# Performance work log

Hardware: AMD Instinct MI355X
Metric: run time of the kernel (lower is better)

## Reference

```python
import jax, jax.numpy as jnp
import numpy as np

PI = float(np.pi)


def _layernorm(x, g, b, eps=1e-5):
    mu = jnp.mean(x, axis=-1, keepdims=True)
    var = jnp.var(x, axis=-1, keepdims=True)
    return (x - mu) * jax.lax.rsqrt(var + eps) * g + b


def setup_inputs() -> dict:
    key = jax.random.key(0)
    B, L, D, P = 4, 2048, 256, 32
    ks = jax.random.split(key, 16)

    def lin_w(k, fi, fo):
        return (jax.random.normal(k, (fi, fo), dtype=jnp.float32) / np.sqrt(fi)).astype(jnp.float32)

    inp = {
        'x': jax.random.normal(ks[0], (B, L, D), dtype=jnp.float32),
        'pos_phases': jax.random.normal(ks[1], (L, P), dtype=jnp.float32) * PI,
        'w_mem1v': lin_w(ks[2], D, P), 'b_mem1v': jnp.zeros((P,), jnp.float32),
        'w_mem1o': lin_w(ks[3], P, D), 'b_mem1o': jnp.zeros((D,), jnp.float32),
        'w_off': lin_w(ks[4], D + P, P), 'b_off': jnp.zeros((P,), jnp.float32),
        'w_key': lin_w(ks[5], D, P), 'b_key': jnp.zeros((P,), jnp.float32),
        'w_val': lin_w(ks[6], D, D), 'b_val': jnp.zeros((D,), jnp.float32),
        'w_sk1': lin_w(ks[7], 2 * D, D), 'b_sk1': jnp.zeros((D,), jnp.float32),
        'w_sk2': lin_w(ks[8], D, P), 'b_sk2': jnp.zeros((P,), jnp.float32),
        'w_gate': lin_w(ks[9], D, 1), 'b_gate': jnp.zeros((1,), jnp.float32),
        'ln_g': jnp.ones((D,), jnp.float32), 'ln_b': jnp.zeros((D,), jnp.float32),
        'w_out': lin_w(ks[10], D, D), 'b_out': jnp.zeros((D,), jnp.float32),
    }
    return inp


def reference(x, pos_phases, w_mem1v, b_mem1v, w_mem1o, b_mem1o, w_off, b_off,
              w_key, b_key, w_val, b_val, w_sk1, b_sk1, w_sk2, b_sk2,
              w_gate, b_gate, ln_g, ln_b, w_out, b_out):
    B, L, D = x.shape
    P = pos_phases.shape[-1]

    pos_cos = jnp.cos(pos_phases)  # [L,P]
    pos_sin = jnp.sin(pos_phases)

    # Memory 1: flat [B,L,P] phasor cumulative memory
    v1 = x @ w_mem1v + b_mem1v                       # [B,L,P]
    mem1_cos = jnp.cumsum(pos_cos[None] * v1, axis=1)
    mem1_sin = jnp.cumsum(pos_sin[None] * v1, axis=1)

    offset_input = jnp.concatenate([x, jnp.broadcast_to(pos_phases[None], (B, L, P))], axis=-1)
    offset = jnp.tanh(offset_input @ w_off + b_off) * PI
    oc, os = jnp.cos(offset), jnp.sin(offset)
    query_cos = pos_cos[None] * oc - pos_sin[None] * os
    query_sin = pos_sin[None] * oc + pos_cos[None] * os
    pos_ret = (mem1_cos * query_cos + mem1_sin * query_sin) / np.sqrt(P)
    pos_out = pos_ret @ w_mem1o + b_mem1o            # [B,L,D]

    # Memory 2: full [B,L,P,D] phasor KV cumulative memory
    key_phases = jnp.tanh(x @ w_key + b_key) * PI    # [B,L,P]
    key_cos, key_sin = jnp.cos(key_phases), jnp.sin(key_phases)
    values = x @ w_val + b_val                       # [B,L,D]
    store_gate = jax.nn.sigmoid(x @ w_gate + b_gate) # [B,L,1]

    positions = jnp.arange(1, L + 1, dtype=x.dtype)[None, :, None]
    context_avg = jnp.cumsum(x, axis=1) / positions
    h = jax.nn.gelu(jnp.concatenate([x, context_avg], axis=-1) @ w_sk1 + b_sk1, approximate=False)
    storage_phases = jnp.tanh(h @ w_sk2 + b_sk2) * PI  # [B,L,P]

    gated_v = values * store_gate                    # [B,L,D]
    kv_mem_cos = jnp.cumsum(jnp.cos(storage_phases)[..., None] * gated_v[:, :, None, :], axis=1)  # [B,L,P,D]
    kv_mem_sin = jnp.cumsum(jnp.sin(storage_phases)[..., None] * gated_v[:, :, None, :], axis=1)

    gate_cumsum = jnp.clip(jnp.cumsum(store_gate, axis=1), 1.0, None)  # [B,L,1]
    kv_retrieved = jnp.einsum('blpd,blp->bld', kv_mem_cos, key_cos) + \
                   jnp.einsum('blpd,blp->bld', kv_mem_sin, key_sin)
    kv_retrieved = kv_retrieved / (jnp.sqrt(gate_cumsum) * np.sqrt(P))

    combined = pos_out + kv_retrieved
    return x + _layernorm(combined, ln_g, ln_b) @ w_out + b_out
```

## Files before the change

kernel.cpp:

```cpp
#include <hip/hip_runtime.h>
#include <hip/hip_bf16.h>

constexpr int B_ = 4;
constexpr int L_ = 2048;
constexpr int D_ = 256;
constexpr int P_ = 32;
constexpr int CL = 32;
constexpr int NC = L_ / CL;

#define PI_F 3.14159265358979323846f
#define INV_SQRT_P 0.17677669529663687f

typedef __attribute__((ext_vector_type(8))) short short8_t;
typedef __attribute__((ext_vector_type(4))) float floatx4;

static __device__ inline short f2bf(float f) {
  unsigned int u;
  __builtin_memcpy(&u, &f, 4);
  unsigned int r = (u + 0x7fffu + ((u >> 16) & 1u)) >> 16;
  return (short)r;
}
static __device__ inline float bf2f(short s) {
  unsigned int u = ((unsigned int)(unsigned short)s) << 16;
  float f;
  __builtin_memcpy(&f, &u, 4);
  return f;
}

__global__ void wprep(const float* __restrict__ x, const float* __restrict__ pos,
                      const float* __restrict__ w_val, const float* __restrict__ w_mem1v,
                      const float* __restrict__ w_off, const float* __restrict__ b_off,
                      const float* __restrict__ w_key, const float* __restrict__ w_gate,
                      const float* __restrict__ w_sk1, const float* __restrict__ w_out,
                      const float* __restrict__ w_sk2, const float* __restrict__ w_mem1o,
                      short* __restrict__ WA, short* __restrict__ W1,
                      short* __restrict__ WO, short* __restrict__ W2T,
                      short* __restrict__ W1OT,
                      short* __restrict__ xbf, float* __restrict__ poff,
                      float* __restrict__ ctxsum) {
  __shared__ float2 psum[2][128];
  int blk = blockIdx.x, tid = threadIdx.x;
  if (blk < 384) {
    int idx = blk * 256 + tid;
    int n = idx >> 8, k = idx & 255;
    float v;
    if (n < 256) v = w_val[k * 256 + n];
    else if (n < 288) v = w_mem1v[k * 32 + (n - 256)];
    else if (n < 320) v = w_off[k * 32 + (n - 288)];
    else if (n < 352) v = w_key[k * 32 + (n - 320)];
    else if (n == 352) v = w_gate[k];
    else v = 0.f;
    WA[idx] = f2bf(v);
  } else if (blk < 896) {
    int idx = (blk - 384) * 256 + tid;
    int n = idx >> 9, k = idx & 511;
    W1[idx] = f2bf(w_sk1[k * 256 + n]);
  } else if (blk < 1152) {
    int idx = (blk - 896) * 256 + tid;
    int n = idx >> 8, k = idx & 255;
    WO[idx] = f2bf(w_out[k * 256 + n]);
  } else if (blk < 1184) {
    int idx = (blk - 1152) * 256 + tid;
    int p = idx >> 8, k = idx & 255;
    W2T[idx] = f2bf(w_sk2[k * 32 + p]);
  } else if (blk < 1216) {
    int idx = (blk - 1184) * 256 + tid;
    int d = idx >> 5, p = idx & 31;
    W1OT[idx] = f2bf(w_mem1o[p * 256 + d]);
  } else if (blk < 1472) {
    int idx = (blk - 1216) * 256 + tid;
    int l = idx >> 5, p = idx & 31;
    float a = b_off[p];
#pragma unroll 8
    for (int j = 0; j < 32; ++j) a += pos[l * 32 + j] * w_off[(256 + j) * 32 + p];
    poff[idx] = a;
  } else {
    int c2 = blk - 1472;
    int b = c2 >> 6, ch = c2 & 63;
    int d2 = (tid & 127) * 2, h = tid >> 7;
    int tokb = b * L_ + ch * 32 + h * 16;
    float2 xv[16];
#pragma unroll
    for (int i = 0; i < 16; ++i)
      xv[i] = *(const float2*)&x[(tokb + i) * 256 + d2];
    float2 s = {0.f, 0.f};
#pragma unroll
    for (int i = 0; i < 16; ++i) { s.x += xv[i].x; s.y += xv[i].y; }
#pragma unroll
    for (int i = 0; i < 16; ++i) {
      short2 o;
      o.x = f2bf(xv[i].x);
      o.y = f2bf(xv[i].y);
      *(short2*)&xbf[(tokb + i) * 256 + d2] = o;
    }
    psum[h][tid & 127] = s;
    __syncthreads();
    if (h == 0) {
      float2 o = psum[1][tid & 127];
      float2 tot = {s.x + o.x, s.y + o.y};
      *(float2*)&ctxsum[c2 * 256 + d2] = tot;
    }
  }
}

__global__ __launch_bounds__(384, 3) void gemmA3(const short* __restrict__ xbf,
                                                 const short* __restrict__ WA,
                                                 const float* __restrict__ pos,
                                                 const float* __restrict__ poff,
                                                 const float* __restrict__ b_mem1v,
                                                 const float* __restrict__ b_key,
                                                 const float* __restrict__ b_gate,
                                                 const float* __restrict__ b_val,
                                                 float* __restrict__ m1cT,
                                                 float* __restrict__ m1sT,
                                                 float* __restrict__ qc,
                                                 float* __restrict__ qs,
                                                 short* __restrict__ K2bf,
                                                 short* __restrict__ gvT,
                                                 float* __restrict__ sg) {
  __shared__ float YL[16][132];
  __shared__ float gsh[16];
  int tid = threadIdx.x;
  int lane = tid & 63, w = tid >> 6;
  int ml = lane & 15, quad = lane >> 4, kq = quad * 8;
  int bc = blockIdx.x;
  int bc32 = bc >> 1, half = bc & 1;
  int tok0 = bc * 16;
  floatx4 acc[4] = {};
  const short* A0p = &xbf[(tok0 + ml) * 256 + kq];
  const short* Bp = &WA[(w * 64 + ml) * 256 + kq];
#pragma unroll
  for (int ks = 0; ks < 8; ++ks) {
    short8_t a0 = *(const short8_t*)(A0p + ks * 32);
#pragma unroll
    for (int nt = 0; nt < 4; ++nt) {
      short8_t b = *(const short8_t*)(Bp + nt * 16 * 256 + ks * 32);
      acc[nt] = __builtin_amdgcn_mfma_f32_16x16x32_bf16(a0, b, acc[nt], 0, 0, 0);
    }
  }
  if (w >= 4) {
#pragma unroll
    for (int nt = 0; nt < 4; ++nt) {
      int col = (w - 4) * 64 + nt * 16 + ml;
#pragma unroll
      for (int r = 0; r < 4; ++r)
        YL[quad * 4 + r][col] = acc[nt][r];
    }
  }
  __syncthreads();
  if (tid < 256) {
#pragma unroll
    for (int it = 0; it < 2; ++it) {
      int idx = it * 256 + tid;
      int t = idx >> 5, p = idx & 31;
      int tok = tok0 + t, l = tok & (L_ - 1);
      int b = tok >> 11;
      float v1 = YL[t][p] + b_mem1v[p];
      float ph = pos[l * 32 + p];
      float pc = cosf(ph), ps = sinf(ph);
      int idxT = (b * 32 + p) * L_ + l;
      m1cT[idxT] = pc * v1;
      m1sT[idxT] = ps * v1;
      float off = tanhf(YL[t][32 + p] + poff[l * 32 + p]) * PI_F;
      float oc = cosf(off), os = sinf(off);
      int gidx = tok * 32 + p;
      qc[gidx] = pc * oc - ps * os;
      qs[gidx] = ps * oc + pc * os;
      float kp = tanhf(YL[t][64 + p] + b_key[p]) * PI_F;
      K2bf[tok * 64 + p] = f2bf(cosf(kp));
      K2bf[tok * 64 + 32 + p] = f2bf(sinf(kp));
      if (p == 0) {
        float g = 1.f / (1.f + expf(-(YL[t][96] + b_gate[0])));
        sg[tok] = g;
        gsh[t] = g;
      }
    }
  }
  __syncthreads();
  if (w < 4) {
#pragma unroll
    for (int nt = 0; nt < 4; ++nt) {
      int d = w * 64 + nt * 16 + ml;
      float bv = b_val[d];
      int t0 = quad * 4;
      short4 o;
      o.x = f2bf((acc[nt][0] + bv) * gsh[t0 + 0]);
      o.y = f2bf((acc[nt][1] + bv) * gsh[t0 + 1]);
      o.z = f2bf((acc[nt][2] + bv) * gsh[t0 + 2]);
      o.w = f2bf((acc[nt][3] + bv) * gsh[t0 + 3]);
      *(short4*)&gvT[(bc32 * 256 + d) * 32 + half * 16 + t0] = o;
    }
  }
}

__global__ void scan_all(float* __restrict__ m1cT, float* __restrict__ m1sT,
                         float* __restrict__ sg) {
  __shared__ float wsum[4];
  int blk = blockIdx.x;
  int tid = threadIdx.x;
  int lane = tid & 63, w = tid >> 6;
  float* arr;
  int base;
  if (blk < 256) {
    arr = (blk < 128) ? m1cT : m1sT;
    base = (blk & 127) * L_;
  } else {
    arr = sg;
    base = (blk - 256) * L_;
  }
  int sbase = base + w * 512;
  float v[8];
#pragma unroll
  for (int i = 0; i < 8; ++i) v[i] = arr[sbase + i * 64 + lane];
  float carry = 0.f;
#pragma unroll
  for (int i = 0; i < 8; ++i) {
    float vv = v[i];
#pragma unroll
    for (int off = 1; off < 64; off <<= 1) {
      float n = __shfl_up(vv, off, 64);
      if (lane >= off) vv += n;
    }
    vv += carry;
    v[i] = vv;
    carry = __shfl(vv, 63, 64);
  }
  if (lane == 0) wsum[w] = carry;
  __syncthreads();
  float off = 0.f;
  for (int ww = 0; ww < w; ++ww) off += wsum[ww];
#pragma unroll
  for (int i = 0; i < 8; ++i) arr[sbase + i * 64 + lane] = v[i] + off;
}

union __align__(16) CDMem {
  short As[32][520];
  struct { short HS[32][280]; short SPL[64][40]; } h;
};
__global__ __launch_bounds__(512, 4) void gemmCD(const short* __restrict__ xbf,
                                                 const float* __restrict__ x,
                                                 const float* __restrict__ ctxsum,
                                                 const short* __restrict__ W1,
                                                 const float* __restrict__ b_sk1,
                                                 const short* __restrict__ W2T,
                                                 const float* __restrict__ b_sk2,
                                                 const short* __restrict__ gvT,
                                                 short* __restrict__ SPbf,
                                                 short* __restrict__ UT) {
  __shared__ CDMem sm;
  __shared__ float stmp[256];
  int tid = threadIdx.x;
  int bc = blockIdx.x;
  int tok0 = bc * 32;
  int bI = bc >> 6, ch = bc & 63;
  int lane = tid & 63, w = tid >> 6;
  int ml = lane & 15, quad = lane >> 4, kq = quad * 8;
#pragma unroll
  for (int pass = 0; pass < 2; ++pass) {
    int idx = pass * 512 + tid;
    int row = idx >> 5, c8 = idx & 31;
    *(short8_t*)&sm.As[row][c8 * 8] =
        *(const short8_t*)&xbf[(tok0 + row) * 256 + c8 * 8];
  }
  {
    int d = tid & 255, h = tid >> 8;
    float cp = 0.f;
    int sb = bI * 64 * 256 + d;
    int c = 0;
    for (; c + 8 <= ch; c += 8) {
      float t0 = ctxsum[sb + (c + 0) * 256];
      float t1 = ctxsum[sb + (c + 1) * 256];
      float t2 = ctxsum[sb + (c + 2) * 256];
      float t3 = ctxsum[sb + (c + 3) * 256];
      float t4 = ctxsum[sb + (c + 4) * 256];
      float t5 = ctxsum[sb + (c + 5) * 256];
      float t6 = ctxsum[sb + (c + 6) * 256];
      float t7 = ctxsum[sb + (c + 7) * 256];
      cp += ((t0 + t1) + (t2 + t3)) + ((t4 + t5) + (t6 + t7));
    }
    for (; c < ch; ++c) cp += ctxsum[sb + c * 256];
    float xv[16];
    int xb = (tok0 + h * 16) * 256 + d;
#pragma unroll
    for (int i = 0; i < 16; ++i) xv[i] = x[xb + i * 256];
    float p = 0.f;
#pragma unroll
    for (int i = 0; i < 16; ++i) p += xv[i];
    if (h == 0) stmp[d] = p;
    __syncthreads();
    float run = cp + (h ? stmp[d] : 0.f);
    int l0 = ch * 32 + h * 16;
#pragma unroll
    for (int i = 0; i < 16; ++i) {
      run += xv[i];
      sm.As[h * 16 + i][256 + d] = f2bf(run / (float)(l0 + i + 1));
    }
  }
  __syncthreads();
  int n0w = w * 32;
  floatx4 acc[2][2] = {};
#pragma unroll
  for (int kt = 0; kt < 16; ++kt) {
    short8_t a0 = *(short8_t*)&sm.As[ml][kt * 32 + kq];
    short8_t a1 = *(short8_t*)&sm.As[16 + ml][kt * 32 + kq];
    short8_t b0 = *(const short8_t*)&W1[(n0w + ml) * 512 + kt * 32 + kq];
    short8_t b1 = *(const short8_t*)&W1[(n0w + 16 + ml) * 512 + kt * 32 + kq];
    acc[0][0] = __builtin_amdgcn_mfma_f32_16x16x32_bf16(a0, b0, acc[0][0], 0, 0, 0);
    acc[0][1] = __builtin_amdgcn_mfma_f32_16x16x32_bf16(a0, b1, acc[0][1], 0, 0, 0);
    acc[1][0] = __builtin_amdgcn_mfma_f32_16x16x32_bf16(a1, b0, acc[1][0], 0, 0, 0);
    acc[1][1] = __builtin_amdgcn_mfma_f32_16x16x32_bf16(a1, b1, acc[1][1], 0, 0, 0);
  }
  short hv[2][2][4];
#pragma unroll
  for (int nt = 0; nt < 2; ++nt) {
    float bv = b_sk1[n0w + nt * 16 + ml];
#pragma unroll
    for (int mt = 0; mt < 2; ++mt)
#pragma unroll
      for (int r = 0; r < 4; ++r) {
        float v = acc[mt][nt][r] + bv;
        float g = 0.5f * v * (1.f + erff(v * 0.70710678118654752f));
        hv[mt][nt][r] = f2bf(g);
      }
  }
  __syncthreads();
#pragma unroll
  for (int mt = 0; mt < 2; ++mt)
#pragma unroll
    for (int nt = 0; nt < 2; ++nt)
#pragma unroll
      for (int r = 0; r < 4; ++r)
        sm.h.HS[mt * 16 + quad * 4 + r][n0w + nt * 16 + ml] = hv[mt][nt][r];
  __syncthreads();
  if (w < 4) {
    int th = w & 1, ph = w >> 1;
    floatx4 pacc = {};
#pragma unroll
    for (int s = 0; s < 8; ++s) {
      short8_t a = *(short8_t*)&sm.h.HS[th * 16 + ml][s * 32 + kq];
      short8_t b0 = *(const short8_t*)&W2T[(ph * 16 + ml) * 256 + s * 32 + kq];
      pacc = __builtin_amdgcn_mfma_f32_16x16x32_bf16(a, b0, pacc, 0, 0, 0);
    }
    int p = ph * 16 + ml;
    float bs = b_sk2[p];
#pragma unroll
    for (int r = 0; r < 4; ++r) {
      int tl = th * 16 + quad * 4 + r;
      int tok = tok0 + tl;
      float sp = tanhf(pacc[r] + bs) * PI_F;
      short c = f2bf(cosf(sp)), s2 = f2bf(sinf(sp));
      sm.h.SPL[p][tl] = c;
      sm.h.SPL[32 + p][tl] = s2;
      SPbf[tok * 64 + p] = c;
      SPbf[tok * 64 + 32 + p] = s2;
    }
  }
  __syncthreads();
  short8_t a[4];
#pragma unroll
  for (int mt = 0; mt < 4; ++mt) a[mt] = *(short8_t*)&sm.h.SPL[mt * 16 + ml][kq];
  floatx4 acc3[4][2] = {};
#pragma unroll
  for (int nt = 0; nt < 2; ++nt) {
    int d = w * 32 + nt * 16 + ml;
    short8_t b = *(const short8_t*)&gvT[(bc * 256 + d) * 32 + kq];
#pragma unroll
    for (int mt = 0; mt < 4; ++mt)
      acc3[mt][nt] = __builtin_amdgcn_mfma_f32_16x16x32_bf16(a[mt], b, acc3[mt][nt], 0, 0, 0);
  }
#pragma unroll
  for (int mt = 0; mt < 4; ++mt)
#pragma unroll
    for (int nt = 0; nt < 2; ++nt) {
      int d = w * 32 + nt * 16 + ml;
      short4 o;
      o.x = f2bf(acc3[mt][nt][0]);
      o.y = f2bf(acc3[mt][nt][1]);
      o.z = f2bf(acc3[mt][nt][2]);
      o.w = f2bf(acc3[mt][nt][3]);
      *(short4*)&UT[(bc * 256 + d) * 64 + mt * 16 + quad * 4] = o;
    }
}

__global__ void kernelE(short* __restrict__ UT) {
  int t = blockIdx.x * 256 + threadIdx.x;
  int pi = t >> 1, half = t & 1;
  int q = pi & 63;
  int d = (pi >> 6) & 255;
  int b = pi >> 14;
  const int cs = 256 * 64;
  int base = ((b * NC) * 256 + d) * 64 + q + half * 32 * cs;
  short v[32];
#pragma unroll
  for (int c = 0; c < 32; ++c) v[c] = UT[base + c * cs];
  float tot = 0.f;
#pragma unroll
  for (int c = 0; c < 32; ++c) tot += bf2f(v[c]);
  float other = __shfl_xor(tot, 1, 64);
  float run = half ? other : 0.f;
#pragma unroll
  for (int c = 0; c < 32; ++c) {
    UT[base + c * cs] = f2bf(run);
    run += bf2f(v[c]);
  }
}

struct __align__(16) FGMem {
  short SL[32][40];
  short PR[32][40];
  float CMB[32][260];
  short CBN[32][280];
  float LG[256], LB[256];
  float scl[32], mu_s[32], rs_s[32];
};
__global__ __launch_bounds__(512, 4) void fgOut(const short* __restrict__ UT,
                                                const short* __restrict__ SPbf,
                                                const short* __restrict__ K2bf,
                                                const short* __restrict__ gvT,
                                                const float* __restrict__ sgc,
                                                const float* __restrict__ m1cT,
                                                const float* __restrict__ m1sT,
                                                const float* __restrict__ qc,
                                                const float* __restrict__ qs,
                                                const short* __restrict__ W1OT,
                                                const float* __restrict__ b_mem1o,
                                                const float* __restrict__ ln_g,
                                                const float* __restrict__ ln_b,
                                                const short* __restrict__ WO,
                                                const float* __restrict__ b_out,
                                                const float* __restrict__ x,
                                                float* __restrict__ out) {
  __shared__ FGMem sm;
  int tid5 = threadIdx.x;
  int bc = blockIdx.x;
  int lbase = bc * CL;
  int bb = bc >> 6, lloc = (bc & 63) * 32;
  int lane = tid5 & 63, w = tid5 >> 6;
  int ml = lane & 15, quad = lane >> 4, kq = quad * 8;
  int d0 = w * 32;
  if (tid5 < 32) sm.scl[tid5] = rsqrtf(fmaxf(sgc[lbase + tid5], 1.f)) * INV_SQRT_P;
  if (tid5 >= 256) {
    int d = tid5 - 256;
    sm.LG[d] = ln_g[d];
    sm.LB[d] = ln_b[d];
  }
  short8_t ka0 = *(const short8_t*)&K2bf[(lbase + ml) * 64 + kq];
  short8_t ka1 = *(const short8_t*)&K2bf[(lbase + 16 + ml) * 64 + kq];
  short8_t kb0 = *(const short8_t*)&K2bf[(lbase + ml) * 64 + 32 + kq];
  short8_t kb1 = *(const short8_t*)&K2bf[(lbase + 16 + ml) * 64 + 32 + kq];
  if (w == 0) {
    floatx4 sacc[2][2] = {};
#pragma unroll
    for (int ks2 = 0; ks2 < 2; ++ks2) {
      short8_t a0 = (ks2 == 0) ? ka0 : kb0;
      short8_t a1 = (ks2 == 0) ? ka1 : kb1;
      short8_t b0 = *(const short8_t*)&SPbf[(lbase + ml) * 64 + ks2 * 32 + kq];
      short8_t b1 = *(const short8_t*)&SPbf[(lbase + 16 + ml) * 64 + ks2 * 32 + kq];
      sacc[0][0] = __builtin_amdgcn_mfma_f32_16x16x32_bf16(a0, b0, sacc[0][0], 0, 0, 0);
      sacc[0][1] = __builtin_amdgcn_mfma_f32_16x16x32_bf16(a0, b1, sacc[0][1], 0, 0, 0);
      sacc[1][0] = __builtin_amdgcn_mfma_f32_16x16x32_bf16(a1, b0, sacc[1][0], 0, 0, 0);
      sacc[1][1] = __builtin_amdgcn_mfma_f32_16x16x32_bf16(a1, b1, sacc[1][1], 0, 0, 0);
    }
#pragma unroll
    for (int mt = 0; mt < 2; ++mt)
#pragma unroll
      for (int nt = 0; nt < 2; ++nt)
#pragma unroll
        for (int r = 0; r < 4; ++r) {
          int trow = mt * 16 + quad * 4 + r;
          int scol = nt * 16 + ml;
          float v = (scol <= trow) ? sacc[mt][nt][r] : 0.f;
          sm.SL[trow][scol] = f2bf(v);
        }
  } else {
    int t7 = tid5 - 64;
    for (int i = t7; i < 1024; i += 448) {
      int pp = i >> 5, t = i & 31;
      int gT = (bb * 32 + pp) * L_ + lloc + t;
      int g = (lbase + t) * 32 + pp;
      sm.PR[t][pp] = f2bf((m1cT[gT] * qc[g] + m1sT[gT] * qs[g]) * INV_SQRT_P);
    }
  }
  __syncthreads();
  floatx4 acc[2][2] = {};
#pragma unroll
  for (int nt = 0; nt < 2; ++nt) {
    short8_t b0 = *(const short8_t*)&UT[(bc * 256 + d0 + nt * 16 + ml) * 64 + kq];
    short8_t b1 = *(const short8_t*)&UT[(bc * 256 + d0 + nt * 16 + ml) * 64 + 32 + kq];
    acc[0][nt] = __builtin_amdgcn_mfma_f32_16x16x32_bf16(ka0, b0, acc[0][nt], 0, 0, 0);
    acc[1][nt] = __builtin_amdgcn_mfma_f32_16x16x32_bf16(ka1, b0, acc[1][nt], 0, 0, 0);
    acc[0][nt] = __builtin_amdgcn_mfma_f32_16x16x32_bf16(kb0, b1, acc[0][nt], 0, 0, 0);
    acc[1][nt] = __builtin_amdgcn_mfma_f32_16x16x32_bf16(kb1, b1, acc[1][nt], 0, 0, 0);
  }
  {
    short8_t a0 = *(short8_t*)&sm.SL[ml][kq];
    short8_t a1 = *(short8_t*)&sm.SL[16 + ml][kq];
#pragma unroll
    for (int nt = 0; nt < 2; ++nt) {
      short8_t b = *(const short8_t*)&gvT[(bc * 256 + d0 + nt * 16 + ml) * 32 + kq];
      acc[0][nt] = __builtin_amdgcn_mfma_f32_16x16x32_bf16(a0, b, acc[0][nt], 0, 0, 0);
      acc[1][nt] = __builtin_amdgcn_mfma_f32_16x16x32_bf16(a1, b, acc[1][nt], 0, 0, 0);
    }
  }
  floatx4 macc[2][2] = {};
  {
    short8_t a0 = *(short8_t*)&sm.PR[ml][kq];
    short8_t a1 = *(short8_t*)&sm.PR[16 + ml][kq];
#pragma unroll
    for (int nt = 0; nt < 2; ++nt) {
      short8_t b = *(const short8_t*)&W1OT[(d0 + nt * 16 + ml) * 32 + kq];
      macc[0][nt] = __builtin_amdgcn_mfma_f32_16x16x32_bf16(a0, b, macc[0][nt], 0, 0, 0);
      macc[1][nt] = __builtin_amdgcn_mfma_f32_16x16x32_bf16(a1, b, macc[1][nt], 0, 0, 0);
    }
  }
#pragma unroll
  for (int mt = 0; mt < 2; ++mt)
#pragma unroll
    for (int nt = 0; nt < 2; ++nt) {
      int d = d0 + nt * 16 + ml;
      float bm = b_mem1o[d];
#pragma unroll
      for (int r = 0; r < 4; ++r) {
        int t = mt * 16 + quad * 4 + r;
        sm.CMB[t][d] = acc[mt][nt][r] * sm.scl[t] + macc[mt][nt][r] + bm;
      }
    }
  __syncthreads();
  {
    int t = tid5 >> 4, g = tid5 & 15;
    float s = 0.f, s2 = 0.f;
#pragma unroll
    for (int j = 0; j < 16; ++j) {
      float v = sm.CMB[t][g + j * 16];
      s += v;
      s2 += v * v;
    }
#pragma unroll
    for (int m = 1; m < 16; m <<= 1) {
      s += __shfl_xor(s, m, 64);
      s2 += __shfl_xor(s2, m, 64);
    }
    if (g == 0) {
      float mu = s / (float)D_;
      float var = s2 / (float)D_ - mu * mu;
      sm.mu_s[t] = mu;
      sm.rs_s[t] = rsqrtf(var + 1e-5f);
    }
  }
  __syncthreads();
#pragma unroll
  for (int it = 0; it < 16; ++it) {
    int i = it * 512 + tid5;
    int t = i >> 8, d = i & 255;
    sm.CBN[t][d] = f2bf((sm.CMB[t][d] - sm.mu_s[t]) * sm.rs_s[t] * sm.LG[d] + sm.LB[d]);
  }
  __syncthreads();
  floatx4 acc2[2][2] = {};
#pragma unroll
  for (int kt = 0; kt < 8; ++kt) {
    short8_t a0 = *(short8_t*)&sm.CBN[ml][kt * 32 + kq];
    short8_t a1 = *(short8_t*)&sm.CBN[16 + ml][kt * 32 + kq];
#pragma unroll
    for (int nt = 0; nt < 2; ++nt) {
      short8_t b = *(const short8_t*)&WO[(d0 + nt * 16 + ml) * 256 + kt * 32 + kq];
      acc2[0][nt] = __builtin_amdgcn_mfma_f32_16x16x32_bf16(a0, b, acc2[0][nt], 0, 0, 0);
      acc2[1][nt] = __builtin_amdgcn_mfma_f32_16x16x32_bf16(a1, b, acc2[1][nt], 0, 0, 0);
    }
  }
#pragma unroll
  for (int nt = 0; nt < 2; ++nt) {
    int n = d0 + nt * 16 + ml;
    float bv = b_out[n];
#pragma unroll
    for (int mt = 0; mt < 2; ++mt)
#pragma unroll
      for (int r = 0; r < 4; ++r) {
        int tok = lbase + mt * 16 + quad * 4 + r;
        out[tok * 256 + n] = x[tok * 256 + n] + acc2[mt][nt][r] + bv;
      }
  }
}

extern "C" void kernel_launch(void* const* d_in, const int* in_sizes, int n_in,
                              void* d_out, int out_size, void* d_ws, size_t ws_size,
                              hipStream_t stream) {
  const float* x = (const float*)d_in[0];
  const float* pos = (const float*)d_in[1];
  const float* w_mem1v = (const float*)d_in[2];
  const float* b_mem1v = (const float*)d_in[3];
  const float* w_mem1o = (const float*)d_in[4];
  const float* b_mem1o = (const float*)d_in[5];
  const float* w_off = (const float*)d_in[6];
  const float* b_off = (const float*)d_in[7];
  const float* w_key = (const float*)d_in[8];
  const float* b_key = (const float*)d_in[9];
  const float* w_val = (const float*)d_in[10];
  const float* b_val = (const float*)d_in[11];
  const float* w_sk1 = (const float*)d_in[12];
  const float* b_sk1 = (const float*)d_in[13];
  const float* w_sk2 = (const float*)d_in[14];
  const float* b_sk2 = (const float*)d_in[15];
  const float* w_gate = (const float*)d_in[16];
  const float* b_gate = (const float*)d_in[17];
  const float* ln_g = (const float*)d_in[18];
  const float* ln_b = (const float*)d_in[19];
  const float* w_out = (const float*)d_in[20];
  const float* b_out = (const float*)d_in[21];
  float* out = (float*)d_out;
  float* ws = (float*)d_ws;

  const int BLP = B_ * L_ * P_;
  const int BLD = B_ * L_ * D_;
  float* m1cT = ws;
  float* m1sT = m1cT + BLP;
  float* qc = m1sT + BLP;
  float* qs = qc + BLP;
  float* sg = qs + BLP;
  float* poff = sg + B_ * L_;
  float* ctxsum = poff + L_ * P_;
  short* UT = (short*)(ctxsum + B_ * 64 * 256);
  short* xbf = UT + (size_t)B_ * NC * 256 * 64;
  short* ctxbf = xbf + BLD;
  short* hs = ctxbf + BLD;
  short* gvT = hs + BLD;
  short* K2bf = gvT + BLD;
  short* SPbf = K2bf + B_ * L_ * 64;
  short* WA = SPbf + B_ * L_ * 64;
  short* W1 = WA + 384 * 256;
  short* WO = W1 + 256 * 512;
  short* W2T = WO + 256 * 256;
  short* W1OT = W2T + 32 * 256;

  wprep<<<1728, 256, 0, stream>>>(x, pos, w_val, w_mem1v, w_off, b_off, w_key, w_gate,
                                  w_sk1, w_out, w_sk2, w_mem1o, WA, W1, WO, W2T, W1OT,
                                  xbf, poff, ctxsum);
  gemmA3<<<512, 384, 0, stream>>>(xbf, WA, pos, poff, b_mem1v, b_key, b_gate, b_val,
                                  m1cT, m1sT, qc, qs, K2bf, gvT, sg);
  gemmCD<<<256, 512, 0, stream>>>(xbf, x, ctxsum, W1, b_sk1, W2T, b_sk2, gvT, SPbf, UT);
  kernelE<<<512, 256, 0, stream>>>(UT);
  scan_all<<<260, 256, 0, stream>>>(m1cT, m1sT, sg);
  fgOut<<<256, 512, 0, stream>>>(UT, SPbf, K2bf, gvT, sg, m1cT, m1sT, qc, qs,
                                 W1OT, b_mem1o, ln_g, ln_b, WO, b_out, x, out);
}
```

Measured before the change: 168.7 us.

## Double threads per block across kernels and pre-scan chunk context sums

gemmA3, gemmCD and fgOut each use twice as many waves, with every wave covering half as many output columns. kernelE now splits each prefix over four lanes instead of two. The serial loop in gemmCD that summed preceding chunk totals is replaced by an exclusive scan of ctxsum, done in extra blocks of scan_all, which now runs before gemmCD. The aim is more parallelism and latency hiding on a grid of only 256–512 blocks, at the cost of less register reuse per wave and heavier 1024-thread blocks.

New measurement: 166.1 us. About the same (-1.5%).

```diff
diff --git a/kernel.cpp b/kernel.cpp
--- a/kernel.cpp
+++ b/kernel.cpp
@@ -103,7 +103,7 @@
   }
 }
 
-__global__ __launch_bounds__(384, 3) void gemmA3(const short* __restrict__ xbf,
+__global__ __launch_bounds__(768, 6) void gemmA3(const short* __restrict__ xbf,
                                                  const short* __restrict__ WA,
                                                  const float* __restrict__ pos,
                                                  const float* __restrict__ poff,
@@ -126,61 +126,57 @@
   int bc = blockIdx.x;
   int bc32 = bc >> 1, half = bc & 1;
   int tok0 = bc * 16;
-  floatx4 acc[4] = {};
+  floatx4 acc[2] = {};
   const short* A0p = &xbf[(tok0 + ml) * 256 + kq];
-  const short* Bp = &WA[(w * 64 + ml) * 256 + kq];
+  const short* Bp = &WA[(w * 32 + ml) * 256 + kq];
 #pragma unroll
   for (int ks = 0; ks < 8; ++ks) {
     short8_t a0 = *(const short8_t*)(A0p + ks * 32);
 #pragma unroll
-    for (int nt = 0; nt < 4; ++nt) {
+    for (int nt = 0; nt < 2; ++nt) {
       short8_t b = *(const short8_t*)(Bp + nt * 16 * 256 + ks * 32);
       acc[nt] = __builtin_amdgcn_mfma_f32_16x16x32_bf16(a0, b, acc[nt], 0, 0, 0);
     }
   }
-  if (w >= 4) {
-#pragma unroll
-    for (int nt = 0; nt < 4; ++nt) {
-      int col = (w - 4) * 64 + nt * 16 + ml;
+  if (w >= 8) {
+#pragma unroll
+    for (int nt = 0; nt < 2; ++nt) {
+      int col = (w - 8) * 32 + nt * 16 + ml;
 #pragma unroll
       for (int r = 0; r < 4; ++r)
         YL[quad * 4 + r][col] = acc[nt][r];
     }
   }
   __syncthreads();
-  if (tid < 256) {
-#pragma unroll
-    for (int it = 0; it < 2; ++it) {
-      int idx = it * 256 + tid;
-      int t = idx >> 5, p = idx & 31;
-      int tok = tok0 + t, l = tok & (L_ - 1);
-      int b = tok >> 11;
-      float v1 = YL[t][p] + b_mem1v[p];
-      float ph = pos[l * 32 + p];
-      float pc = cosf(ph), ps = sinf(ph);
-      int idxT = (b * 32 + p) * L_ + l;
-      m1cT[idxT] = pc * v1;
-      m1sT[idxT] = ps * v1;
-      float off = tanhf(YL[t][32 + p] + poff[l * 32 + p]) * PI_F;
-      float oc = cosf(off), os = sinf(off);
-      int gidx = tok * 32 + p;
-      qc[gidx] = pc * oc - ps * os;
-      qs[gidx] = ps * oc + pc * os;
-      float kp = tanhf(YL[t][64 + p] + b_key[p]) * PI_F;
-      K2bf[tok * 64 + p] = f2bf(cosf(kp));
-      K2bf[tok * 64 + 32 + p] = f2bf(sinf(kp));
-      if (p == 0) {
-        float g = 1.f / (1.f + expf(-(YL[t][96] + b_gate[0])));
-        sg[tok] = g;
-        gsh[t] = g;
-      }
-    }
-  }
-  __syncthreads();
-  if (w < 4) {
-#pragma unroll
-    for (int nt = 0; nt < 4; ++nt) {
-      int d = w * 64 + nt * 16 + ml;
+  if (tid < 512) {
+    int t = tid >> 5, p = tid & 31;
+    int tok = tok0 + t, l = tok & (L_ - 1);
+    int b = tok >> 11;
+    float v1 = YL[t][p] + b_mem1v[p];
+    float ph = pos[l * 32 + p];
+    float pc = cosf(ph), ps = sinf(ph);
+    int idxT = (b * 32 + p) * L_ + l;
+    m1cT[idxT] = pc * v1;
+    m1sT[idxT] = ps * v1;
+    float off = tanhf(YL[t][32 + p] + poff[l * 32 + p]) * PI_F;
+    float oc = cosf(off), os = sinf(off);
+    int gidx = tok * 32 + p;
+    qc[gidx] = pc * oc - ps * os;
+    qs[gidx] = ps * oc + pc * os;
+    float kp = tanhf(YL[t][64 + p] + b_key[p]) * PI_F;
+    K2bf[tok * 64 + p] = f2bf(cosf(kp));
+    K2bf[tok * 64 + 32 + p] = f2bf(sinf(kp));
+    if (p == 0) {
+      float g = 1.f / (1.f + expf(-(YL[t][96] + b_gate[0])));
+      sg[tok] = g;
+      gsh[t] = g;
+    }
+  }
+  __syncthreads();
+  if (w < 8) {
+#pragma unroll
+    for (int nt = 0; nt < 2; ++nt) {
+      int d = w * 32 + nt * 16 + ml;
       float bv = b_val[d];
       int t0 = quad * 4;
       short4 o;
@@ -194,10 +190,24 @@
 }
 
 __global__ void scan_all(float* __restrict__ m1cT, float* __restrict__ m1sT,
-                         float* __restrict__ sg) {
-  __shared__ float wsum[4];
+                         float* __restrict__ sg, float* __restrict__ ctxsum) {
   int blk = blockIdx.x;
   int tid = threadIdx.x;
+  if (blk >= 260) {
+    int b = blk - 260;
+    int base = b * 64 * 256 + tid;
+    float v[64];
+#pragma unroll
+    for (int c = 0; c < 64; ++c) v[c] = ctxsum[base + c * 256];
+    float run = 0.f;
+#pragma unroll
+    for (int c = 0; c < 64; ++c) {
+      ctxsum[base + c * 256] = run;
+      run += v[c];
+    }
+    return;
+  }
+  __shared__ float wsum[4];
   int lane = tid & 63, w = tid >> 6;
   float* arr;
   int base;
@@ -237,100 +247,79 @@
   short As[32][520];
   struct { short HS[32][280]; short SPL[64][40]; } h;
 };
-__global__ __launch_bounds__(512, 4) void gemmCD(const short* __restrict__ xbf,
-                                                 const float* __restrict__ x,
-                                                 const float* __restrict__ ctxsum,
-                                                 const short* __restrict__ W1,
-                                                 const float* __restrict__ b_sk1,
-                                                 const short* __restrict__ W2T,
-                                                 const float* __restrict__ b_sk2,
-                                                 const short* __restrict__ gvT,
-                                                 short* __restrict__ SPbf,
-                                                 short* __restrict__ UT) {
+__global__ __launch_bounds__(1024, 4) void gemmCD(const short* __restrict__ xbf,
+                                                  const float* __restrict__ x,
+                                                  const float* __restrict__ ctxsum,
+                                                  const short* __restrict__ W1,
+                                                  const float* __restrict__ b_sk1,
+                                                  const short* __restrict__ W2T,
+                                                  const float* __restrict__ b_sk2,
+                                                  const short* __restrict__ gvT,
+                                                  short* __restrict__ SPbf,
+                                                  short* __restrict__ UT) {
   __shared__ CDMem sm;
-  __shared__ float stmp[256];
+  __shared__ float stmp[4][256];
   int tid = threadIdx.x;
   int bc = blockIdx.x;
   int tok0 = bc * 32;
   int bI = bc >> 6, ch = bc & 63;
   int lane = tid & 63, w = tid >> 6;
   int ml = lane & 15, quad = lane >> 4, kq = quad * 8;
-#pragma unroll
-  for (int pass = 0; pass < 2; ++pass) {
-    int idx = pass * 512 + tid;
-    int row = idx >> 5, c8 = idx & 31;
+  {
+    int row = tid >> 5, c8 = tid & 31;
     *(short8_t*)&sm.As[row][c8 * 8] =
         *(const short8_t*)&xbf[(tok0 + row) * 256 + c8 * 8];
   }
   {
-    int d = tid & 255, h = tid >> 8;
-    float cp = 0.f;
-    int sb = bI * 64 * 256 + d;
-    int c = 0;
-    for (; c + 8 <= ch; c += 8) {
-      float t0 = ctxsum[sb + (c + 0) * 256];
-      float t1 = ctxsum[sb + (c + 1) * 256];
-      float t2 = ctxsum[sb + (c + 2) * 256];
-      float t3 = ctxsum[sb + (c + 3) * 256];
-      float t4 = ctxsum[sb + (c + 4) * 256];
-      float t5 = ctxsum[sb + (c + 5) * 256];
-      float t6 = ctxsum[sb + (c + 6) * 256];
-      float t7 = ctxsum[sb + (c + 7) * 256];
-      cp += ((t0 + t1) + (t2 + t3)) + ((t4 + t5) + (t6 + t7));
-    }
-    for (; c < ch; ++c) cp += ctxsum[sb + c * 256];
-    float xv[16];
-    int xb = (tok0 + h * 16) * 256 + d;
-#pragma unroll
-    for (int i = 0; i < 16; ++i) xv[i] = x[xb + i * 256];
+    int d = tid & 255, qh = tid >> 8;
+    float cp = ctxsum[(bI * 64 + ch) * 256 + d];
+    float xv[8];
+    int xb = (tok0 + qh * 8) * 256 + d;
+#pragma unroll
+    for (int i = 0; i < 8; ++i) xv[i] = x[xb + i * 256];
     float p = 0.f;
 #pragma unroll
-    for (int i = 0; i < 16; ++i) p += xv[i];
-    if (h == 0) stmp[d] = p;
+    for (int i = 0; i < 8; ++i) p += xv[i];
+    stmp[qh][d] = p;
     __syncthreads();
-    float run = cp + (h ? stmp[d] : 0.f);
-    int l0 = ch * 32 + h * 16;
-#pragma unroll
-    for (int i = 0; i < 16; ++i) {
+    float run = cp;
+    for (int j = 0; j < qh; ++j) run += stmp[j][d];
+    int l0 = ch * 32 + qh * 8;
+#pragma unroll
+    for (int i = 0; i < 8; ++i) {
       run += xv[i];
-      sm.As[h * 16 + i][256 + d] = f2bf(run / (float)(l0 + i + 1));
-    }
-  }
-  __syncthreads();
-  int n0w = w * 32;
-  floatx4 acc[2][2] = {};
+      sm.As[qh * 8 + i][256 + d] = f2bf(run / (float)(l0 + i + 1));
+    }
+  }
+  __syncthreads();
+  int n0w = w * 16;
+  floatx4 acc[2] = {};
 #pragma unroll
   for (int kt = 0; kt < 16; ++kt) {
     short8_t a0 = *(short8_t*)&sm.As[ml][kt * 32 + kq];
     short8_t a1 = *(short8_t*)&sm.As[16 + ml][kt * 32 + kq];
     short8_t b0 = *(const short8_t*)&W1[(n0w + ml) * 512 + kt * 32 + kq];
-    short8_t b1 = *(const short8_t*)&W1[(n0w + 16 + ml) * 512 + kt * 32 + kq];
-    acc[0][0] = __builtin_amdgcn_mfma_f32_16x16x32_bf16(a0, b0, acc[0][0], 0, 0, 0);
-    acc[0][1] = __builtin_amdgcn_mfma_f32_16x16x32_bf16(a0, b1, acc[0][1], 0, 0, 0);
-    acc[1][0] = __builtin_amdgcn_mfma_f32_16x16x32_bf16(a1, b0, acc[1][0], 0, 0, 0);
-    acc[1][1] = __builtin_amdgcn_mfma_f32_16x16x32_bf16(a1, b1, acc[1][1], 0, 0, 0);
-  }
-  short hv[2][2][4];
-#pragma unroll
-  for (int nt = 0; nt < 2; ++nt) {
-    float bv = b_sk1[n0w + nt * 16 + ml];
+    acc[0] = __builtin_amdgcn_mfma_f32_16x16x32_bf16(a0, b0, acc[0], 0, 0, 0);
+    acc[1] = __builtin_amdgcn_mfma_f32_16x16x32_bf16(a1, b0, acc[1], 0, 0, 0);
+  }
+  short hv[2][4];
+  {
+    float bv = b_sk1[n0w + ml];
 #pragma unroll
     for (int mt = 0; mt < 2; ++mt)
 #pragma unroll
       for (int r = 0; r < 4; ++r) {
-        float v = acc[mt][nt][r] + bv;
+        float v = acc[mt][r] + bv;
         float g = 0.5f * v * (1.f + erff(v * 0.70710678118654752f));
-        hv[mt][nt][r] = f2bf(g);
+        hv[mt][r] = f2bf(g);
       }
   }
   __syncthreads();
 #pragma unroll
   for (int mt = 0; mt < 2; ++mt)
 #pragma unroll
-    for (int nt = 0; nt < 2; ++nt)
-#pragma unroll
-      for (int r = 0; r < 4; ++r)
-        sm.h.HS[mt * 16 + quad * 4 + r][n0w + nt * 16 + ml] = hv[mt][nt][r];
+    for (int r = 0; r < 4; ++r)
+      sm.h.HS[mt * 16 + quad * 4 + r][n0w + ml] = hv[mt][r];
   __syncthreads();
   if (w < 4) {
     int th = w & 1, ph = w >> 1;
@@ -359,47 +348,48 @@
   short8_t a[4];
 #pragma unroll
   for (int mt = 0; mt < 4; ++mt) a[mt] = *(short8_t*)&sm.h.SPL[mt * 16 + ml][kq];
-  floatx4 acc3[4][2] = {};
-#pragma unroll
-  for (int nt = 0; nt < 2; ++nt) {
-    int d = w * 32 + nt * 16 + ml;
+  floatx4 acc3[4] = {};
+  {
+    int d = w * 16 + ml;
     short8_t b = *(const short8_t*)&gvT[(bc * 256 + d) * 32 + kq];
 #pragma unroll
     for (int mt = 0; mt < 4; ++mt)
-      acc3[mt][nt] = __builtin_amdgcn_mfma_f32_16x16x32_bf16(a[mt], b, acc3[mt][nt], 0, 0, 0);
-  }
-#pragma unroll
-  for (int mt = 0; mt < 4; ++mt)
-#pragma unroll
-    for (int nt = 0; nt < 2; ++nt) {
-      int d = w * 32 + nt * 16 + ml;
-      short4 o;
-      o.x = f2bf(acc3[mt][nt][0]);
-      o.y = f2bf(acc3[mt][nt][1]);
-      o.z = f2bf(acc3[mt][nt][2]);
-      o.w = f2bf(acc3[mt][nt][3]);
-      *(short4*)&UT[(bc * 256 + d) * 64 + mt * 16 + quad * 4] = o;
-    }
+      acc3[mt] = __builtin_amdgcn_mfma_f32_16x16x32_bf16(a[mt], b, acc3[mt], 0, 0, 0);
+  }
+#pragma unroll
+  for (int mt = 0; mt < 4; ++mt) {
+    int d = w * 16 + ml;
+    short4 o;
+    o.x = f2bf(acc3[mt][0]);
+    o.y = f2bf(acc3[mt][1]);
+    o.z = f2bf(acc3[mt][2]);
+    o.w = f2bf(acc3[mt][3]);
+    *(short4*)&UT[(bc * 256 + d) * 64 + mt * 16 + quad * 4] = o;
+  }
 }
 
 __global__ void kernelE(short* __restrict__ UT) {
   int t = blockIdx.x * 256 + threadIdx.x;
-  int pi = t >> 1, half = t & 1;
+  int pi = t >> 2, j = t & 3;
   int q = pi & 63;
   int d = (pi >> 6) & 255;
   int b = pi >> 14;
   const int cs = 256 * 64;
-  int base = ((b * NC) * 256 + d) * 64 + q + half * 32 * cs;
-  short v[32];
-#pragma unroll
-  for (int c = 0; c < 32; ++c) v[c] = UT[base + c * cs];
+  int base = ((b * NC) * 256 + d) * 64 + q + j * 16 * cs;
+  short v[16];
+#pragma unroll
+  for (int c = 0; c < 16; ++c) v[c] = UT[base + c * cs];
   float tot = 0.f;
 #pragma unroll
-  for (int c = 0; c < 32; ++c) tot += bf2f(v[c]);
-  float other = __shfl_xor(tot, 1, 64);
-  float run = half ? other : 0.f;
-#pragma unroll
-  for (int c = 0; c < 32; ++c) {
+  for (int c = 0; c < 16; ++c) tot += bf2f(v[c]);
+  int lane = threadIdx.x & 63;
+  int gb = lane & ~3;
+  float t0 = __shfl(tot, gb + 0, 64);
+  float t1 = __shfl(tot, gb + 1, 64);
+  float t2 = __shfl(tot, gb + 2, 64);
+  float run = (j > 0 ? t0 : 0.f) + (j > 1 ? t1 : 0.f) + (j > 2 ? t2 : 0.f);
+#pragma unroll
+  for (int c = 0; c < 16; ++c) {
     UT[base + c * cs] = f2bf(run);
     run += bf2f(v[c]);
   }
@@ -413,23 +403,23 @@
   float LG[256], LB[256];
   float scl[32], mu_s[32], rs_s[32];
 };
-__global__ __launch_bounds__(512, 4) void fgOut(const short* __restrict__ UT,
-                                                const short* __restrict__ SPbf,
-                                                const short* __restrict__ K2bf,
-                                                const short* __restrict__ gvT,
-                                                const float* __restrict__ sgc,
-                                                const float* __restrict__ m1cT,
-                                                const float* __restrict__ m1sT,
-                                                const float* __restrict__ qc,
-                                                const float* __restrict__ qs,
-                                                const short* __restrict__ W1OT,
-                                                const float* __restrict__ b_mem1o,
-                                                const float* __restrict__ ln_g,
-                                                const float* __restrict__ ln_b,
-                                                const short* __restrict__ WO,
-                                                const float* __restrict__ b_out,
-                                                const float* __restrict__ x,
-                                                float* __restrict__ out) {
+__global__ __launch_bounds__(1024, 4) void fgOut(const short* __restrict__ UT,
+                                                 const short* __restrict__ SPbf,
+                                                 const short* __restrict__ K2bf,
+                                                 const short* __restrict__ gvT,
+                                                 const float* __restrict__ sgc,
+                                                 const float* __restrict__ m1cT,
+                                                 const float* __restrict__ m1sT,
+                                                 const float* __restrict__ qc,
+                                                 const float* __restrict__ qs,
+                                                 const short* __restrict__ W1OT,
+                                                 const float* __restrict__ b_mem1o,
+                                                 const float* __restrict__ ln_g,
+                                                 const float* __restrict__ ln_b,
+                                                 const short* __restrict__ WO,
+                                                 const float* __restrict__ b_out,
+                                                 const float* __restrict__ x,
+                                                 float* __restrict__ out) {
   __shared__ FGMem sm;
   int tid5 = threadIdx.x;
   int bc = blockIdx.x;
@@ -437,9 +427,9 @@
   int bb = bc >> 6, lloc = (bc & 63) * 32;
   int lane = tid5 & 63, w = tid5 >> 6;
   int ml = lane & 15, quad = lane >> 4, kq = quad * 8;
-  int d0 = w * 32;
+  int d0 = w * 16;
   if (tid5 < 32) sm.scl[tid5] = rsqrtf(fmaxf(sgc[lbase + tid5], 1.f)) * INV_SQRT_P;
-  if (tid5 >= 256) {
+  if (tid5 >= 256 && tid5 < 512) {
     int d = tid5 - 256;
     sm.LG[d] = ln_g[d];
     sm.LB[d] = ln_b[d];
@@ -474,7 +464,7 @@
         }
   } else {
     int t7 = tid5 - 64;
-    for (int i = t7; i < 1024; i += 448) {
+    for (int i = t7; i < 1024; i += 960) {
       int pp = i >> 5, t = i & 31;
       int gT = (bb * 32 + pp) * L_ + lloc + t;
       int g = (lbase + t) * 32 + pp;
@@ -482,61 +472,53 @@
     }
   }
   __syncthreads();
-  floatx4 acc[2][2] = {};
-#pragma unroll
-  for (int nt = 0; nt < 2; ++nt) {
-    short8_t b0 = *(const short8_t*)&UT[(bc * 256 + d0 + nt * 16 + ml) * 64 + kq];
-    short8_t b1 = *(const short8_t*)&UT[(bc * 256 + d0 + nt * 16 + ml) * 64 + 32 + kq];
-    acc[0][nt] = __builtin_amdgcn_mfma_f32_16x16x32_bf16(ka0, b0, acc[0][nt], 0, 0, 0);
-    acc[1][nt] = __builtin_amdgcn_mfma_f32_16x16x32_bf16(ka1, b0, acc[1][nt], 0, 0, 0);
-    acc[0][nt] = __builtin_amdgcn_mfma_f32_16x16x32_bf16(kb0, b1, acc[0][nt], 0, 0, 0);
-    acc[1][nt] = __builtin_amdgcn_mfma_f32_16x16x32_bf16(kb1, b1, acc[1][nt], 0, 0, 0);
+  floatx4 acc[2] = {};
+  {
+    short8_t b0 = *(const short8_t*)&UT[(bc * 256 + d0 + ml) * 64 + kq];
+    short8_t b1 = *(const short8_t*)&UT[(bc * 256 + d0 + ml) * 64 + 32 + kq];
+    acc[0] = __builtin_amdgcn_mfma_f32_16x16x32_bf16(ka0, b0, acc[0], 0, 0, 0);
+    acc[1] = __builtin_amdgcn_mfma_f32_16x16x32_bf16(ka1, b0, acc[1], 0, 0, 0);
+    acc[0] = __builtin_amdgcn_mfma_f32_16x16x32_bf16(kb0, b1, acc[0], 0, 0, 0);
+    acc[1] = __builtin_amdgcn_mfma_f32_16x16x32_bf16(kb1, b1, acc[1], 0, 0, 0);
   }
   {
     short8_t a0 = *(short8_t*)&sm.SL[ml][kq];
     short8_t a1 = *(short8_t*)&sm.SL[16 + ml][kq];
-#pragma unroll
-    for (int nt = 0; nt < 2; ++nt) {
-      short8_t b = *(const short8_t*)&gvT[(bc * 256 + d0 + nt * 16 + ml) * 32 + kq];
-      acc[0][nt] = __builtin_amdgcn_mfma_f32_16x16x32_bf16(a0, b, acc[0][nt], 0, 0, 0);
-      acc[1][nt] = __builtin_amdgcn_mfma_f32_16x16x32_bf16(a1, b, acc[1][nt], 0, 0, 0);
-    }
-  }
-  floatx4 macc[2][2] = {};
+    short8_t b = *(const short8_t*)&gvT[(bc * 256 + d0 + ml) * 32 + kq];
+    acc[0] = __builtin_amdgcn_mfma_f32_16x16x32_bf16(a0, b, acc[0], 0, 0, 0);
+    acc[1] = __builtin_amdgcn_mfma_f32_16x16x32_bf16(a1, b, acc[1], 0, 0, 0);
+  }
+  floatx4 macc[2] = {};
   {
     short8_t a0 = *(short8_t*)&sm.PR[ml][kq];
     short8_t a1 = *(short8_t*)&sm.PR[16 + ml][kq];
-#pragma unroll
-    for (int nt = 0; nt < 2; ++nt) {
-      short8_t b = *(const short8_t*)&W1OT[(d0 + nt * 16 + ml) * 32 + kq];
-      macc[0][nt] = __builtin_amdgcn_mfma_f32_16x16x32_bf16(a0, b, macc[0][nt], 0, 0, 0);
-      macc[1][nt] = __builtin_amdgcn_mfma_f32_16x16x32_bf16(a1, b, macc[1][nt], 0, 0, 0);
-    }
-  }
-#pragma unroll
-  for (int mt = 0; mt < 2; ++mt)
-#pragma unroll
-    for (int nt = 0; nt < 2; ++nt) {
-      int d = d0 + nt * 16 + ml;
-      float bm = b_mem1o[d];
+    short8_t b = *(const short8_t*)&W1OT[(d0 + ml) * 32 + kq];
+    macc[0] = __builtin_amdgcn_mfma_f32_16x16x32_bf16(a0, b, macc[0], 0, 0, 0);
+    macc[1] = __builtin_amdgcn_mfma_f32_16x16x32_bf16(a1, b, macc[1], 0, 0, 0);
+  }
+  {
+    int d = d0 + ml;
+    float bm = b_mem1o[d];
+#pragma unroll
+    for (int mt = 0; mt < 2; ++mt)
 #pragma unroll
       for (int r = 0; r < 4; ++r) {
         int t = mt * 16 + quad * 4 + r;
-        sm.CMB[t][d] = acc[mt][nt][r] * sm.scl[t] + macc[mt][nt][r] + bm;
+        sm.CMB[t][d] = acc[mt][r] * sm.scl[t] + macc[mt][r] + bm;
       }
-    }
-  __syncthreads();
-  {
-    int t = tid5 >> 4, g = tid5 & 15;
+  }
+  __syncthreads();
+  {
+    int t = tid5 >> 5, g = tid5 & 31;
     float s = 0.f, s2 = 0.f;
 #pragma unroll
-    for (int j = 0; j < 16; ++j) {
-      float v = sm.CMB[t][g + j * 16];
+    for (int j = 0; j < 8; ++j) {
+      float v = sm.CMB[t][g + j * 32];
       s += v;
       s2 += v * v;
     }
 #pragma unroll
-    for (int m = 1; m < 16; m <<= 1) {
+    for (int m = 1; m < 32; m <<= 1) {
       s += __shfl_xor(s, m, 64);
       s2 += __shfl_xor(s2, m, 64);
     }
@@ -549,34 +531,30 @@
   }
   __syncthreads();
 #pragma unroll
-  for (int it = 0; it < 16; ++it) {
-    int i = it * 512 + tid5;
+  for (int it = 0; it < 8; ++it) {
+    int i = it * 1024 + tid5;
     int t = i >> 8, d = i & 255;
     sm.CBN[t][d] = f2bf((sm.CMB[t][d] - sm.mu_s[t]) * sm.rs_s[t] * sm.LG[d] + sm.LB[d]);
   }
   __syncthreads();
-  floatx4 acc2[2][2] = {};
+  floatx4 acc2[2] = {};
 #pragma unroll
   for (int kt = 0; kt < 8; ++kt) {
     short8_t a0 = *(short8_t*)&sm.CBN[ml][kt * 32 + kq];
     short8_t a1 = *(short8_t*)&sm.CBN[16 + ml][kt * 32 + kq];
-#pragma unroll
-    for (int nt = 0; nt < 2; ++nt) {
-      short8_t b = *(const short8_t*)&WO[(d0 + nt * 16 + ml) * 256 + kt * 32 + kq];
-      acc2[0][nt] = __builtin_amdgcn_mfma_f32_16x16x32_bf16(a0, b, acc2[0][nt], 0, 0, 0);
-      acc2[1][nt] = __builtin_amdgcn_mfma_f32_16x16x32_bf16(a1, b, acc2[1][nt], 0, 0, 0);
-    }
-  }
-#pragma unroll
-  for (int nt = 0; nt < 2; ++nt) {
-    int n = d0 + nt * 16 + ml;
+    short8_t b = *(const short8_t*)&WO[(d0 + ml) * 256 + kt * 32 + kq];
+    acc2[0] = __builtin_amdgcn_mfma_f32_16x16x32_bf16(a0, b, acc2[0], 0, 0, 0);
+    acc2[1] = __builtin_amdgcn_mfma_f32_16x16x32_bf16(a1, b, acc2[1], 0, 0, 0);
+  }
+  {
+    int n = d0 + ml;
     float bv = b_out[n];
 #pragma unroll
     for (int mt = 0; mt < 2; ++mt)
 #pragma unroll
       for (int r = 0; r < 4; ++r) {
         int tok = lbase + mt * 16 + quad * 4 + r;
-        out[tok * 256 + n] = x[tok * 256 + n] + acc2[mt][nt][r] + bv;
+        out[tok * 256 + n] = x[tok * 256 + n] + acc2[mt][r] + bv;
       }
   }
 }
@@ -634,11 +612,11 @@
   wprep<<<1728, 256, 0, stream>>>(x, pos, w_val, w_mem1v, w_off, b_off, w_key, w_gate,
                                   w_sk1, w_out, w_sk2, w_mem1o, WA, W1, WO, W2T, W1OT,
                                   xbf, poff, ctxsum);
-  gemmA3<<<512, 384, 0, stream>>>(xbf, WA, pos, poff, b_mem1v, b_key, b_gate, b_val,
+  gemmA3<<<512, 768, 0, stream>>>(xbf, WA, pos, poff, b_mem1v, b_key, b_gate, b_val,
                                   m1cT, m1sT, qc, qs, K2bf, gvT, sg);
-  gemmCD<<<256, 512, 0, stream>>>(xbf, x, ctxsum, W1, b_sk1, W2T, b_sk2, gvT, SPbf, UT);
-  kernelE<<<512, 256, 0, stream>>>(UT);
-  scan_all<<<260, 256, 0, stream>>>(m1cT, m1sT, sg);
-  fgOut<<<256, 512, 0, stream>>>(UT, SPbf, K2bf, gvT, sg, m1cT, m1sT, qc, qs,
-                                 W1OT, b_mem1o, ln_g, ln_b, WO, b_out, x, out);
-}
+  scan_all<<<264, 256, 0, stream>>>(m1cT, m1sT, sg, ctxsum);
+  gemmCD<<<256, 1024, 0, stream>>>(xbf, x, ctxsum, W1, b_sk1, W2T, b_sk2, gvT, SPbf, UT);
+  kernelE<<<1024, 256, 0, stream>>>(UT);
+  fgOut<<<256, 1024, 0, stream>>>(UT, SPbf, K2bf, gvT, sg, m1cT, m1sT, qc, qs,
+                                  W1OT, b_mem1o, ln_g, ln_b, WO, b_out, x, out);
+}
```
